# Kernel tuning notes

Hardware: AMD Instinct MI355X
Metric: run time of the kernel (lower is better)

## Reference

```python
import jax, jax.numpy as jnp
import numpy as np

EMBED = 1024
N_HEAD = 16
HEAD_DIM = EMBED // N_HEAD


def setup_inputs() -> dict:
    key = jax.random.key(0)
    ks = jax.random.split(key, 9)
    def xavier(k, shape, fan_in, fan_out):
        bound = float(np.sqrt(6.0 / (fan_in + fan_out)))
        return jax.random.uniform(k, shape, jnp.float32, -bound, bound)
    x = jax.random.normal(ks[0], (4, 2048, EMBED), jnp.float32)
    wq = xavier(ks[1], (N_HEAD, EMBED, HEAD_DIM), EMBED, HEAD_DIM)
    wk = xavier(ks[2], (N_HEAD, EMBED, HEAD_DIM), EMBED, HEAD_DIM)
    wv = xavier(ks[3], (N_HEAD, EMBED, HEAD_DIM), EMBED, HEAD_DIM)
    bq = jnp.zeros((N_HEAD, 1, HEAD_DIM), jnp.float32)
    bk = jnp.zeros((N_HEAD, 1, HEAD_DIM), jnp.float32)
    bv = jnp.zeros((N_HEAD, 1, HEAD_DIM), jnp.float32)
    # nn.Linear default init: uniform(-1/sqrt(in), 1/sqrt(in)), weight [out, in]
    bnd = 1.0 / float(np.sqrt(EMBED))
    wo = jax.random.uniform(ks[4], (EMBED, EMBED), jnp.float32, -bnd, bnd)
    bo = jax.random.uniform(ks[5], (EMBED,), jnp.float32, -bnd, bnd)
    return {"x": x, "wq": wq, "bq": bq, "wk": wk, "bk": bk,
            "wv": wv, "bv": bv, "wo": wo, "bo": bo}


def reference(x, wq, bq, wk, bk, wv, bv, wo, bo):
    # per-head projections: [b,s,d] x [h,d,e] -> [b,h,s,e]
    q = jnp.einsum('bsd,hde->bhse', x, wq) + bq
    k = jnp.einsum('bsd,hde->bhse', x, wk) + bk
    v = jnp.einsum('bsd,hde->bhse', x, wv) + bv
    scale = 1.0 / jnp.sqrt(jnp.asarray(q.shape[-1], q.dtype))
    scores = jax.nn.softmax(jnp.einsum('bhse,bhte->bhst', q, k) * scale, axis=-1)
    att = jnp.einsum('bhst,bhte->bhse', scores, v)  # [b,h,s,e]
    b, h, s, e = att.shape
    att = att.transpose(0, 2, 1, 3).reshape(b, s, h * e)
    return att @ wo.T + bo
```

## Files before the change

### kernel.cpp

```cpp
#include <hip/hip_runtime.h>
#include <hip/hip_bf16.h>
#include <stdint.h>

typedef __attribute__((ext_vector_type(8))) short short8;
typedef __attribute__((ext_vector_type(4))) short short4v;
typedef __attribute__((ext_vector_type(4))) float f32x4;
typedef __attribute__((ext_vector_type(4))) float float4v;

#define LOG2E_OVER8 0.18033688011112042f

__device__ __forceinline__ short bf16r(float f) {
  union { float f; uint32_t u; } v; v.f = f;
  uint32_t r = (v.u + 0x7FFFu + ((v.u >> 16) & 1u)) >> 16;
  return (short)r;
}

__device__ __forceinline__ void gload16(const void* g, void* l) {
  __builtin_amdgcn_global_load_lds((const __attribute__((address_space(1))) void*)g,
                                   (__attribute__((address_space(3))) void*)l, 16, 0, 0);
}

__global__ void k_prep(const float* __restrict__ x, const float* __restrict__ wo,
                       const float* __restrict__ wq, const float* __restrict__ wk,
                       const float* __restrict__ wv,
                       short* __restrict__ xb, short* __restrict__ wob,
                       short* __restrict__ wt) {
  __shared__ short tile[64][65];
  int bid = blockIdx.x;
  int tid = threadIdx.x;
  if (bid < 4096) {
    size_t i = ((size_t)bid * 256 + tid) * 8;
    float4v v0 = *(const float4v*)(x + i);
    float4v v1 = *(const float4v*)(x + i + 4);
    short8 o = { bf16r(v0[0]), bf16r(v0[1]), bf16r(v0[2]), bf16r(v0[3]),
                 bf16r(v1[0]), bf16r(v1[1]), bf16r(v1[2]), bf16r(v1[3]) };
    *(short8*)(xb + i) = o;
  } else if (bid < 5120) {
    int i = (bid - 4096) * 256 + tid;
    float4v v = *(const float4v*)(wo + (size_t)i * 4);
    short4v o = { bf16r(v[0]), bf16r(v[1]), bf16r(v[2]), bf16r(v[3]) };
    *(short4v*)(wob + (size_t)i * 4) = o;
  } else {
    int b2 = bid - 5120;
    int kt = b2 & 15, h = (b2 >> 4) & 15, wsel = b2 >> 8;
    const float* src = wsel == 0 ? wq : (wsel == 1 ? wk : wv);
    {
      int e = tid & 63, r4 = tid >> 6;
#pragma unroll
      for (int p = 0; p < 16; ++p) {
        int kk = p * 4 + r4;
        tile[kk][e] = bf16r(src[h * 65536 + (kt * 64 + kk) * 64 + e]);
      }
    }
    __syncthreads();
    {
      int kk = tid & 63, r4 = tid >> 6;
#pragma unroll
      for (int p = 0; p < 16; ++p) {
        int e = p * 4 + r4;
        wt[(size_t)(wsel * 1024 + h * 64 + e) * 1024 + kt * 64 + kk] = tile[kk][e];
      }
    }
  }
}

template<int EPI>
__global__ __launch_bounds__(512, 2) void k_gemm(
    const short* __restrict__ A, const short* __restrict__ Bt,
    const float* __restrict__ b0, const float* __restrict__ b1, const float* __restrict__ b2,
    short* __restrict__ qb, short* __restrict__ kb, short* __restrict__ vtb,
    float* __restrict__ outp) {
  __shared__ short smem[73728];
  int tid = threadIdx.x;
  int l = tid & 63, w = tid >> 6;
  int g = l >> 4, c = l & 15;
  int wr = w >> 1, wc = w & 1;
  const int NBX = (EPI == 0) ? 24 : 8;
  const int nwg = NBX * 32;
  int orig = blockIdx.x + blockIdx.y * NBX;
  int swz = (orig & 7) * (nwg >> 3) + (orig >> 3);
  int m0 = (swz / NBX) * 256, n0 = (swz % NBX) * 128;

  f32x4 acc[4][4];
#pragma unroll
  for (int i = 0; i < 4; ++i)
#pragma unroll
    for (int j = 0; j < 4; ++j) acc[i][j] = (f32x4){0.f, 0.f, 0.f, 0.f};

  int aoff[4][2], boff[4][2];
#pragma unroll
  for (int mi = 0; mi < 4; ++mi) {
    int R = wr * 64 + mi * 16 + c;
#pragma unroll
    for (int ks = 0; ks < 2; ++ks)
      aoff[mi][ks] = R * 64 + (((ks * 4 + g) ^ (R & 7)) * 8);
  }
#pragma unroll
  for (int ni = 0; ni < 4; ++ni) {
    int R = wc * 64 + ni * 16 + c;
#pragma unroll
    for (int ks = 0; ks < 2; ++ks)
      boff[ni][ks] = R * 64 + (((ks * 4 + g) ^ (R & 7)) * 8);
  }

  const short* asrc[4]; int adst[4];
  const short* bsrc[2]; int bdst[2];
#pragma unroll
  for (int i = 0; i < 4; ++i) {
    int ch = i * 512 + tid;
    int row = ch >> 3, cbs = ch & 7;
    int sb = cbs ^ (row & 7);
    asrc[i] = A + (size_t)(m0 + row) * 1024 + sb * 8;
    adst[i] = ch * 8;
  }
#pragma unroll
  for (int i = 0; i < 2; ++i) {
    int ch = i * 512 + tid;
    int row = ch >> 3, cbs = ch & 7;
    int sb = cbs ^ (row & 7);
    bsrc[i] = Bt + (size_t)(n0 + row) * 1024 + sb * 8;
    bdst[i] = ch * 8;
  }

#pragma unroll
  for (int i = 0; i < 4; ++i) gload16(asrc[i], &smem[adst[i]]);
#pragma unroll
  for (int i = 0; i < 2; ++i) gload16(bsrc[i], &smem[49152 + bdst[i]]);
#pragma unroll
  for (int i = 0; i < 4; ++i) gload16(asrc[i] + 64, &smem[16384 + adst[i]]);
#pragma unroll
  for (int i = 0; i < 2; ++i) gload16(bsrc[i] + 64, &smem[49152 + 8192 + bdst[i]]);
  asm volatile("s_waitcnt vmcnt(6)" ::: "memory");
  __builtin_amdgcn_s_barrier();

  int cur = 0;
  for (int kt = 0; kt < 16; ++kt) {
    int stg = cur + 2; if (stg >= 3) stg -= 3;
    const short* Ab = &smem[cur * 16384];
    const short* Bb = &smem[49152 + cur * 8192];
    bool pre = (kt + 2 < 16);
    int ko = (kt + 2) * 64;

    short8 af0[4], bf0[4];
#pragma unroll
    for (int mi = 0; mi < 4; ++mi) af0[mi] = *(const short8*)&Ab[aoff[mi][0]];
#pragma unroll
    for (int ni = 0; ni < 4; ++ni) bf0[ni] = *(const short8*)&Bb[boff[ni][0]];
    if (pre) {
      gload16(asrc[0] + ko, &smem[stg * 16384 + adst[0]]);
      gload16(asrc[1] + ko, &smem[stg * 16384 + adst[1]]);
      gload16(bsrc[0] + ko, &smem[49152 + stg * 8192 + bdst[0]]);
    }
    __builtin_amdgcn_s_setprio(1);
#pragma unroll
    for (int mi = 0; mi < 4; ++mi)
#pragma unroll
      for (int ni = 0; ni < 4; ++ni)
        acc[mi][ni] = __builtin_amdgcn_mfma_f32_16x16x32_bf16(af0[mi], bf0[ni], acc[mi][ni], 0, 0, 0);
    __builtin_amdgcn_s_setprio(0);

    short8 af1[4], bf1[4];
#pragma unroll
    for (int mi = 0; mi < 4; ++mi) af1[mi] = *(const short8*)&Ab[aoff[mi][1]];
#pragma unroll
    for (int ni = 0; ni < 4; ++ni) bf1[ni] = *(const short8*)&Bb[boff[ni][1]];
    if (pre) {
      gload16(asrc[2] + ko, &smem[stg * 16384 + adst[2]]);
      gload16(asrc[3] + ko, &smem[stg * 16384 + adst[3]]);
      gload16(bsrc[1] + ko, &smem[49152 + stg * 8192 + bdst[1]]);
    }
    __builtin_amdgcn_s_setprio(1);
#pragma unroll
    for (int mi = 0; mi < 4; ++mi)
#pragma unroll
      for (int ni = 0; ni < 4; ++ni)
        acc[mi][ni] = __builtin_amdgcn_mfma_f32_16x16x32_bf16(af1[mi], bf1[ni], acc[mi][ni], 0, 0, 0);
    __builtin_amdgcn_s_setprio(0);

    if (kt < 15) {
      if (kt < 14) asm volatile("s_waitcnt vmcnt(6)" ::: "memory");
      else         asm volatile("s_waitcnt vmcnt(0)" ::: "memory");
      __builtin_amdgcn_s_barrier();
    }
    cur = cur + 1; if (cur == 3) cur = 0;
  }

  if (EPI == 0 && n0 >= 2048) {
    __syncthreads();
#pragma unroll
    for (int mi = 0; mi < 4; ++mi)
#pragma unroll
      for (int ni = 0; ni < 4; ++ni) {
        int ln = wc * 64 + ni * 16 + c;
        float bias = b2[(n0 - 2048) + ln];
        int ls0 = wr * 64 + mi * 16 + g * 4;
        int blk = ls0 >> 3;
        int sblk = blk ^ (ln & 31);
        short4v o;
#pragma unroll
        for (int r = 0; r < 4; ++r) o[r] = bf16r(acc[mi][ni][r] + bias);
        *(short4v*)&smem[ln * 256 + sblk * 8 + (ls0 & 7)] = o;
      }
    __syncthreads();
    int b = m0 >> 11, s0g = m0 & 2047;
    int h0 = (n0 - 2048) >> 6;
    int vrow0 = (b * 16 + h0) * 64;
#pragma unroll
    for (int p = 0; p < 8; ++p) {
      int ln = p * 16 + (tid >> 5);
      int L2 = tid & 31;
      int T = L2 >> 3, B = L2 & 7;
      int sa0 = T * 64 + (B >> 2) * 32 + (B & 3) * 4;
      int sb0 = sa0 + 16;
      short4v va = *(const short4v*)&smem[ln * 256 + ((sa0 >> 3) ^ (ln & 31)) * 8 + (sa0 & 7)];
      short4v vb = *(const short4v*)&smem[ln * 256 + ((sb0 >> 3) ^ (ln & 31)) * 8 + (sb0 & 7)];
      short8 v = {va[0], va[1], va[2], va[3], vb[0], vb[1], vb[2], vb[3]};
      *(short8*)&vtb[(size_t)(vrow0 + ln) * 2048 + s0g + L2 * 8] = v;
    }
    return;
  }

#pragma unroll
  for (int mi = 0; mi < 4; ++mi)
#pragma unroll
    for (int ni = 0; ni < 4; ++ni) {
      int n = n0 + wc * 64 + ni * 16 + c;
      if (EPI == 0) {
        int sel = n >> 10, nn = n & 1023;
        int h = nn >> 6, e = nn & 63;
        const float* bp = sel == 0 ? b0 : b1;
        short* dst = sel == 0 ? qb : kb;
        float bias = bp[nn];
        float sc = (sel == 0) ? LOG2E_OVER8 : 1.0f;
#pragma unroll
        for (int r = 0; r < 4; ++r) {
          int m = m0 + wr * 64 + mi * 16 + g * 4 + r;
          int b = m >> 11, s = m & 2047;
          float v = (acc[mi][ni][r] + bias) * sc;
          dst[(size_t)((b * 16 + h) * 2048 + s) * 64 + e] = bf16r(v);
        }
      } else {
        float bias = b0[n];
#pragma unroll
        for (int r = 0; r < 4; ++r) {
          int m = m0 + wr * 64 + mi * 16 + g * 4 + r;
          outp[(size_t)m * 1024 + n] = acc[mi][ni][r] + bias;
        }
      }
    }
}

__global__ __launch_bounds__(256, 4) void k_attn(
    const short* __restrict__ Qb, const short* __restrict__ Kb,
    const short* __restrict__ Vt, short* __restrict__ attb) {
  __shared__ short Ks[2][64 * 64];
  __shared__ short Vs[2][64 * 64];
  int tid = threadIdx.x;
  int l = tid & 63, w = tid >> 6;
  int g = l >> 4, c = l & 15;
  int orig = blockIdx.x + blockIdx.y * 16;
  int swz = (orig & 7) * 128 + (orig >> 3);
  int qt = swz & 15, bh = swz >> 4;
  int q0 = qt * 128 + w * 32;

  const short* Qh = Qb + (size_t)bh * 2048 * 64;
  short8 qf[2][2];
#pragma unroll
  for (int qi = 0; qi < 2; ++qi)
#pragma unroll
    for (int es = 0; es < 2; ++es)
      qf[qi][es] = *(const short8*)&Qh[(size_t)(q0 + qi * 16 + c) * 64 + es * 32 + g * 8];

  int koff[4][2];
#pragma unroll
  for (int mi = 0; mi < 4; ++mi) {
    int row = mi * 16 + c;
    koff[mi][0] = row * 64 + ((g ^ (row & 7)) * 8);
    koff[mi][1] = row * 64 + (((4 + g) ^ (row & 7)) * 8);
  }
  int voff[2][4];
#pragma unroll
  for (int ks = 0; ks < 2; ++ks)
#pragma unroll
    for (int ei = 0; ei < 4; ++ei) {
      int row = ei * 16 + c;
      voff[ks][ei] = row * 64 + (((ks * 4 + g) ^ (row & 7)) * 8);
    }

  const short* kptr[2];
  const short* vptr[2];
  int ldst[2];
#pragma unroll
  for (int i = 0; i < 2; ++i) {
    int ch = w * 128 + i * 64 + l;
    int row = ch >> 3, cbs = ch & 7;
    int sb = cbs ^ (row & 7);
    kptr[i] = Kb + (size_t)(bh * 2048 + row) * 64 + sb * 8;
    vptr[i] = Vt + (size_t)(bh * 64 + row) * 2048 + sb * 8;
    ldst[i] = (w * 128 + i * 64) * 8;
  }

  const f32x4 z4 = (f32x4){0.f, 0.f, 0.f, 0.f};
  f32x4 oacc[4][2];
#pragma unroll
  for (int i = 0; i < 4; ++i) { oacc[i][0] = z4; oacc[i][1] = z4; }
  f32x4 lsum[2] = {z4, z4};

  const short one_bf16 = (short)0x3F80;
  const short8 ones = {one_bf16, one_bf16, one_bf16, one_bf16,
                       one_bf16, one_bf16, one_bf16, one_bf16};

  auto stageKV = [&](int buf) {
#pragma unroll
    for (int i = 0; i < 2; ++i) {
      gload16(kptr[i], &Ks[buf][ldst[i]]);
      gload16(vptr[i], &Vs[buf][ldst[i]]);
      kptr[i] += 64 * 64;
      vptr[i] += 64;
    }
  };

  stageKV(0);
  __syncthreads();

  for (int t = 0; t < 32; ++t) {
    int buf = t & 1;
    if (t + 1 < 32) stageKV(buf ^ 1);

    const short* Kbuf = &Ks[buf][0];
    short8 kf0[4], kf1[4];
#pragma unroll
    for (int mi = 0; mi < 4; ++mi) {
      kf0[mi] = *(const short8*)&Kbuf[koff[mi][0]];
      kf1[mi] = *(const short8*)&Kbuf[koff[mi][1]];
    }
    f32x4 sacc[4][2];
    __builtin_amdgcn_s_setprio(1);
#pragma unroll
    for (int mi = 0; mi < 4; ++mi)
#pragma unroll
      for (int qi = 0; qi < 2; ++qi)
        sacc[mi][qi] = __builtin_amdgcn_mfma_f32_16x16x32_bf16(kf0[mi], qf[qi][0], z4, 0, 0, 0);
#pragma unroll
    for (int mi = 0; mi < 4; ++mi)
#pragma unroll
      for (int qi = 0; qi < 2; ++qi)
        sacc[mi][qi] = __builtin_amdgcn_mfma_f32_16x16x32_bf16(kf1[mi], qf[qi][1], sacc[mi][qi], 0, 0, 0);
    __builtin_amdgcn_s_setprio(0);

    short8 pf[2][2];
#pragma unroll
    for (int qi = 0; qi < 2; ++qi) {
      float p[4][4];
#pragma unroll
      for (int mi = 0; mi < 4; ++mi)
#pragma unroll
        for (int r = 0; r < 4; ++r)
          p[mi][r] = __builtin_amdgcn_exp2f(sacc[mi][qi][r]);
#pragma unroll
      for (int ks = 0; ks < 2; ++ks) {
        union { uint32_t w[4]; short8 s; } pu;
        asm("v_cvt_pk_bf16_f32 %0, %1, %2" : "=v"(pu.w[0]) : "v"(p[ks * 2][0]), "v"(p[ks * 2][1]));
        asm("v_cvt_pk_bf16_f32 %0, %1, %2" : "=v"(pu.w[1]) : "v"(p[ks * 2][2]), "v"(p[ks * 2][3]));
        asm("v_cvt_pk_bf16_f32 %0, %1, %2" : "=v"(pu.w[2]) : "v"(p[ks * 2 + 1][0]), "v"(p[ks * 2 + 1][1]));
        asm("v_cvt_pk_bf16_f32 %0, %1, %2" : "=v"(pu.w[3]) : "v"(p[ks * 2 + 1][2]), "v"(p[ks * 2 + 1][3]));
        pf[qi][ks] = pu.s;
      }
    }

    const short* Vbuf = &Vs[buf][0];
    __builtin_amdgcn_s_setprio(1);
#pragma unroll
    for (int qi = 0; qi < 2; ++qi)
#pragma unroll
      for (int ks = 0; ks < 2; ++ks)
        lsum[qi] = __builtin_amdgcn_mfma_f32_16x16x32_bf16(ones, pf[qi][ks], lsum[qi], 0, 0, 0);
#pragma unroll
    for (int ks = 0; ks < 2; ++ks)
#pragma unroll
      for (int ei = 0; ei < 4; ++ei) {
        short8 vf = *(const short8*)&Vbuf[voff[ks][ei]];
#pragma unroll
        for (int qi = 0; qi < 2; ++qi)
          oacc[ei][qi] = __builtin_amdgcn_mfma_f32_16x16x32_bf16(vf, pf[qi][ks], oacc[ei][qi], 0, 0, 0);
      }
    __builtin_amdgcn_s_setprio(0);

    __syncthreads();
  }

  int b = bh >> 4, h = bh & 15;
#pragma unroll
  for (int qi = 0; qi < 2; ++qi) {
    float inv = 1.0f / lsum[qi][0];
    int s = q0 + qi * 16 + c;
#pragma unroll
    for (int ei = 0; ei < 4; ++ei) {
      short4v o;
#pragma unroll
      for (int r = 0; r < 4; ++r) o[r] = bf16r(oacc[ei][qi][r] * inv);
      *(short4v*)&attb[(size_t)(b * 2048 + s) * 1024 + h * 64 + ei * 16 + g * 4] = o;
    }
  }
}

extern "C" void kernel_launch(void* const* d_in, const int* in_sizes, int n_in,
                              void* d_out, int out_size, void* d_ws, size_t ws_size,
                              hipStream_t stream) {
  const float* x  = (const float*)d_in[0];
  const float* wq = (const float*)d_in[1];
  const float* bq = (const float*)d_in[2];
  const float* wk = (const float*)d_in[3];
  const float* bk = (const float*)d_in[4];
  const float* wv = (const float*)d_in[5];
  const float* bv = (const float*)d_in[6];
  const float* wo = (const float*)d_in[7];
  const float* bo = (const float*)d_in[8];
  float* out = (float*)d_out;

  uint8_t* ws = (uint8_t*)d_ws;
  short* xb  = (short*)(ws);
  short* wt  = (short*)(ws + (16u << 20));
  short* wob = (short*)(ws + (22u << 20));
  short* qb  = (short*)(ws + (24u << 20));
  short* kb  = (short*)(ws + (40u << 20));
  short* vtb = (short*)(ws + (56u << 20));
  short* attb = xb;

  k_prep<<<5888, 256, 0, stream>>>(x, wo, wq, wk, wv, xb, wob, wt);
  k_gemm<0><<<dim3(24, 32), 512, 0, stream>>>(xb, wt, bq, bk, bv, qb, kb, vtb, nullptr);
  k_attn<<<dim3(16, 64), 256, 0, stream>>>(qb, kb, vtb, attb);
  k_gemm<1><<<dim3(8, 32), 512, 0, stream>>>(attb, wob, bo, nullptr, nullptr,
                                             nullptr, nullptr, nullptr, out);
}
```

Before: 155.9 us.

## Store V in MFMA-fragment layout and load V fragments directly from global

The projection epilogue now writes V^T in a pre-tiled layout matching the attention kernel's MFMA operand fragments. The attention kernel then loads V fragments straight from global memory into registers each iteration and no longer stages V through LDS. This halves the LDS footprint and removes V LDS traffic. In exchange every wave re-reads V from global or L2 with no cross-wave sharing, and the load latency is exposed within the iteration.

```diff
diff --git a/kernel.cpp b/kernel.cpp
--- a/kernel.cpp
+++ b/kernel.cpp
@@ -204,18 +204,21 @@
     __syncthreads();
     int b = m0 >> 11, s0g = m0 & 2047;
     int h0 = (n0 - 2048) >> 6;
-    int vrow0 = (b * 16 + h0) * 64;
-#pragma unroll
-    for (int p = 0; p < 8; ++p) {
-      int ln = p * 16 + (tid >> 5);
-      int L2 = tid & 31;
-      int T = L2 >> 3, B = L2 & 7;
+    int t0 = s0g >> 6;
+#pragma unroll
+    for (int i = 0; i < 8; ++i) {
+      int combo = i * 8 + w;
+      int hh = combo >> 5;
+      int T = (combo >> 3) & 3;
+      int B = combo & 7;
+      int ln = hh * 64 + l;
       int sa0 = T * 64 + (B >> 2) * 32 + (B & 3) * 4;
       int sb0 = sa0 + 16;
       short4v va = *(const short4v*)&smem[ln * 256 + ((sa0 >> 3) ^ (ln & 31)) * 8 + (sa0 & 7)];
       short4v vb = *(const short4v*)&smem[ln * 256 + ((sb0 >> 3) ^ (ln & 31)) * 8 + (sb0 & 7)];
       short8 v = {va[0], va[1], va[2], va[3], vb[0], vb[1], vb[2], vb[3]};
-      *(short8*)&vtb[(size_t)(vrow0 + ln) * 2048 + s0g + L2 * 8] = v;
+      size_t row = (size_t)((b * 16 + h0 + hh) * 32 + t0 + T) * 8 + B;
+      *(short8*)&vtb[row * 512 + l * 8] = v;
     }
     return;
   }
@@ -254,7 +257,6 @@
     const short* __restrict__ Qb, const short* __restrict__ Kb,
     const short* __restrict__ Vt, short* __restrict__ attb) {
   __shared__ short Ks[2][64 * 64];
-  __shared__ short Vs[2][64 * 64];
   int tid = threadIdx.x;
   int l = tid & 63, w = tid >> 6;
   int g = l >> 4, c = l & 15;
@@ -278,17 +280,16 @@
     koff[mi][0] = row * 64 + ((g ^ (row & 7)) * 8);
     koff[mi][1] = row * 64 + (((4 + g) ^ (row & 7)) * 8);
   }
-  int voff[2][4];
+
+  const short* vbase = Vt + (size_t)bh * 131072;
+  int voff2[2][4];
 #pragma unroll
   for (int ks = 0; ks < 2; ++ks)
 #pragma unroll
-    for (int ei = 0; ei < 4; ++ei) {
-      int row = ei * 16 + c;
-      voff[ks][ei] = row * 64 + (((ks * 4 + g) ^ (row & 7)) * 8);
-    }
+    for (int ei = 0; ei < 4; ++ei)
+      voff2[ks][ei] = ((ks * 4 + g) * 64 + ei * 16 + c) * 8;
 
   const short* kptr[2];
-  const short* vptr[2];
   int ldst[2];
 #pragma unroll
   for (int i = 0; i < 2; ++i) {
@@ -296,7 +297,6 @@
     int row = ch >> 3, cbs = ch & 7;
     int sb = cbs ^ (row & 7);
     kptr[i] = Kb + (size_t)(bh * 2048 + row) * 64 + sb * 8;
-    vptr[i] = Vt + (size_t)(bh * 64 + row) * 2048 + sb * 8;
     ldst[i] = (w * 128 + i * 64) * 8;
   }
 
@@ -310,22 +310,29 @@
   const short8 ones = {one_bf16, one_bf16, one_bf16, one_bf16,
                        one_bf16, one_bf16, one_bf16, one_bf16};
 
-  auto stageKV = [&](int buf) {
+  auto stageK = [&](int buf) {
 #pragma unroll
     for (int i = 0; i < 2; ++i) {
       gload16(kptr[i], &Ks[buf][ldst[i]]);
-      gload16(vptr[i], &Vs[buf][ldst[i]]);
       kptr[i] += 64 * 64;
-      vptr[i] += 64;
     }
   };
 
-  stageKV(0);
+  stageK(0);
   __syncthreads();
 
   for (int t = 0; t < 32; ++t) {
     int buf = t & 1;
-    if (t + 1 < 32) stageKV(buf ^ 1);
+
+    const short* vtile = vbase + (size_t)t * 4096;
+    short8 vf[2][4];
+#pragma unroll
+    for (int ks = 0; ks < 2; ++ks)
+#pragma unroll
+      for (int ei = 0; ei < 4; ++ei)
+        vf[ks][ei] = *(const short8*)&vtile[voff2[ks][ei]];
+
+    if (t + 1 < 32) stageK(buf ^ 1);
 
     const short* Kbuf = &Ks[buf][0];
     short8 kf0[4], kf1[4];
@@ -368,7 +375,6 @@
       }
     }
 
-    const short* Vbuf = &Vs[buf][0];
     __builtin_amdgcn_s_setprio(1);
 #pragma unroll
     for (int qi = 0; qi < 2; ++qi)
@@ -379,10 +385,9 @@
     for (int ks = 0; ks < 2; ++ks)
 #pragma unroll
       for (int ei = 0; ei < 4; ++ei) {
-        short8 vf = *(const short8*)&Vbuf[voff[ks][ei]];
 #pragma unroll
         for (int qi = 0; qi < 2; ++qi)
-          oacc[ei][qi] = __builtin_amdgcn_mfma_f32_16x16x32_bf16(vf, pf[qi][ks], oacc[ei][qi], 0, 0, 0);
+          oacc[ei][qi] = __builtin_amdgcn_mfma_f32_16x16x32_bf16(vf[ks][ei], pf[qi][ks], oacc[ei][qi], 0, 0, 0);
       }
     __builtin_amdgcn_s_setprio(0);
 
```

After: 320.4 us. 2.06x slower.
